# Kernel optimization log

Hardware: AMD Instinct MI355X
Metric: run time of the kernel (lower is better)

## Reference

```python
import jax, jax.numpy as jnp
import numpy as np

N = 8192
E = 262144
C = 256          # in_channels
OUT = 256        # out_channels
H = 4            # num_heads
DH = C // H      # head dim


def setup_inputs() -> dict:
    key = jax.random.key(0)
    ks = jax.random.split(key, 12)
    stdv = 1.0 / np.sqrt(C)
    inp = {
        "x": jax.random.normal(ks[0], (N, C), dtype=jnp.float32),
        "adj": jax.random.randint(ks[1], (2, E), 0, N, dtype=jnp.int64),
        "weight_local": jax.random.uniform(ks[2], (C, C), jnp.float32, -stdv, stdv),
        # nn.MultiheadAttention packed projections
        "in_proj_w": jax.random.normal(ks[3], (3 * C, C), jnp.float32) * stdv,
        "in_proj_b": jnp.zeros((3 * C,), jnp.float32),
        "out_proj_w": jax.random.normal(ks[4], (C, C), jnp.float32) * stdv,
        "out_proj_b": jnp.zeros((C,), jnp.float32),
        "ln_g": jnp.ones((C,), jnp.float32),
        "ln_b": jnp.zeros((C,), jnp.float32),
        "alpha": jnp.zeros((), jnp.float32),
        "fc_w": jax.random.normal(ks[5], (OUT, C), jnp.float32) * stdv,
        "fc_b": jnp.zeros((OUT,), jnp.float32),
    }
    return inp


def _gcn_conv(x, edge_index):
    # out[col] += (1/sqrt(d[col]*d[row])) * x[row], d = in-degree by col
    row, col = edge_index[0], edge_index[1]
    n = x.shape[0]
    d = jax.ops.segment_sum(jnp.ones((edge_index.shape[1],), x.dtype), col, num_segments=n)
    val = jax.lax.rsqrt(d[col] * d[row])
    val = jnp.where(jnp.isfinite(val), val, 0.0)
    msg = x[row] * val[:, None]                      # [E, C] gather + scale
    return jax.ops.segment_sum(msg, col, num_segments=n)  # [N, C] scatter-add


def _mha(x, in_proj_w, in_proj_b, out_proj_w, out_proj_b):
    # single-batch self-attention over all N nodes
    qkv = x @ in_proj_w.T + in_proj_b                # [N, 3C]
    q, k, v = jnp.split(qkv, 3, axis=-1)
    def heads(t):
        return t.reshape(N, H, DH).transpose(1, 0, 2)  # [H, N, DH]
    q, k, v = heads(q), heads(k), heads(v)
    scores = jnp.einsum("hnd,hmd->hnm", q, k) / np.sqrt(DH)  # [H, N, N]
    attn = jax.nn.softmax(scores, axis=-1)
    out = jnp.einsum("hnm,hmd->hnd", attn, v)        # [H, N, DH]
    out = out.transpose(1, 0, 2).reshape(N, C)
    return out @ out_proj_w.T + out_proj_b


def _layernorm(x, g, b, eps=1e-5):
    mu = jnp.mean(x, axis=-1, keepdims=True)
    var = jnp.var(x, axis=-1, keepdims=True)
    return (x - mu) * jax.lax.rsqrt(var + eps) * g + b


def reference(x, adj, weight_local, in_proj_w, in_proj_b, out_proj_w, out_proj_b,
              ln_g, ln_b, alpha, fc_w, fc_b):
    hi = _gcn_conv(x, adj)
    local_embed = hi @ weight_local                   # [N, C]
    attn_out = _mha(x, in_proj_w, in_proj_b, out_proj_w, out_proj_b)
    global_embed = _layernorm(x + attn_out, ln_g, ln_b)
    w = jax.nn.sigmoid(alpha)
    combined = w * local_embed + (1.0 - w) * global_embed
    return combined @ fc_w.T + fc_b                   # [N, OUT]
```

## Files before the change

### kernel.cpp

```cpp
#include <hip/hip_runtime.h>
#include <hip/hip_bf16.h>
#include <math.h>

#define NN   8192
#define EE   262144
#define CC   256
#define HH   4

typedef __bf16 bf16;
typedef __bf16 bf16x8 __attribute__((ext_vector_type(8)));
typedef __bf16 bf16x4 __attribute__((ext_vector_type(4)));
typedef __bf16 bf16x2 __attribute__((ext_vector_type(2)));
typedef float  f32x4  __attribute__((ext_vector_type(4)));

static __device__ __forceinline__ bf16 f2bf(float f) { return (bf16)f; }

static __device__ __forceinline__ unsigned pk2(float a, float b) {
    __hip_bfloat162 h = __float22bfloat162_rn(float2{a, b});
    return *reinterpret_cast<unsigned*>(&h);
}

__global__ void prep_all(const float* __restrict__ x, bf16* __restrict__ xb,
                         const float* __restrict__ ipw, const float* __restrict__ opw,
                         const float* __restrict__ fcw, const float* __restrict__ wloc,
                         bf16* __restrict__ ipwb, bf16* __restrict__ opwb,
                         bf16* __restrict__ fcwb, bf16* __restrict__ wlTb,
                         const int* __restrict__ adj, int* __restrict__ ideg) {
    int b = blockIdx.x, t = threadIdx.x;
    if (b < 2048) {
        for (int i = b * 256 + t; i < NN * CC; i += 2048 * 256) xb[i] = f2bf(x[i]);
    } else if (b < 2816) { int i = (b - 2048) * 256 + t; ipwb[i] = f2bf(ipw[i]); }
    else if (b < 3072)   { int i = (b - 2816) * 256 + t; opwb[i] = f2bf(opw[i]); }
    else if (b < 3328)   { int i = (b - 3072) * 256 + t; fcwb[i] = f2bf(fcw[i]); }
    else if (b < 3584)   { int n = b - 3328;             wlTb[n * 256 + t] = f2bf(wloc[t * 256 + n]); }
    else {
        int e = (b - 3584) * 256 + t;
        if (e < EE) atomicAdd(&ideg[adj[EE + e]], 1);
    }
}

__global__ __launch_bounds__(256) void build_kv(const bf16* __restrict__ qkv,
                                                bf16* __restrict__ Kpk,
                                                bf16* __restrict__ Vpk) {
    __shared__ bf16 tl[64][72];
    const int bx = blockIdx.x;
    const int h  = blockIdx.y;
    const int tid = threadIdx.x;
    #pragma unroll
    for (int i = 0; i < 2; i++) {
        int u = tid + i * 256;
        int key = u >> 3, g = u & 7;
        *reinterpret_cast<bf16x8*>(&tl[key][g * 8]) =
            *reinterpret_cast<const bf16x8*>(qkv + (size_t)(bx * 64 + key) * 768 + 256 + h * 64 + g * 8);
    }
    __syncthreads();
    #pragma unroll
    for (int i = 0; i < 2; i++) {
        int ee = tid + i * 256;
        int l15 = ee & 15, quad = (ee >> 4) & 3, c = (ee >> 6) & 1, ktl = ee >> 7;
        int key_local = (ktl >> 1) * 32 + (l15 >> 2) * 8 + (ktl & 1) * 4 + (l15 & 3);
        bf16x8 v = *reinterpret_cast<const bf16x8*>(&tl[key_local][c * 32 + quad * 8]);
        *reinterpret_cast<bf16x8*>(Kpk + ((size_t)((h * 512 + bx * 4 + ktl) * 2 + c)) * 512
                                       + (quad * 16 + l15) * 8) = v;
    }
    __syncthreads();
    #pragma unroll
    for (int i = 0; i < 2; i++) {
        int u = tid + i * 256;
        int key = u >> 3, g = u & 7;
        *reinterpret_cast<bf16x8*>(&tl[key][g * 8]) =
            *reinterpret_cast<const bf16x8*>(qkv + (size_t)(bx * 64 + key) * 768 + 512 + h * 64 + g * 8);
    }
    __syncthreads();
    #pragma unroll
    for (int i = 0; i < 2; i++) {
        int ee = tid + i * 256;
        int l15 = ee & 15, quad = (ee >> 4) & 3, nt = (ee >> 6) & 3, kcl = ee >> 8;
        bf16x8 v;
        #pragma unroll
        for (int j = 0; j < 8; j++) v[j] = tl[kcl * 32 + quad * 8 + j][nt * 16 + l15];
        *reinterpret_cast<bf16x8*>(Vpk + ((size_t)((h * 256 + bx * 2 + kcl) * 4 + nt)) * 512
                                       + (quad * 16 + l15) * 8) = v;
    }
}

__global__ __launch_bounds__(256) void scan_offsets(const int* __restrict__ ideg,
        int* __restrict__ off, int* __restrict__ cursor, float* __restrict__ rs) {
    __shared__ int ps[256];
    const int tid = threadIdx.x;
    const int base = tid * 32;
    int loc[32];
    int s = 0;
    #pragma unroll
    for (int i = 0; i < 32; i++) { loc[i] = s; s += ideg[base + i]; }
    ps[tid] = s;
    __syncthreads();
    for (int d = 1; d < 256; d <<= 1) {
        int v = (tid >= d) ? ps[tid - d] : 0;
        __syncthreads();
        ps[tid] += v;
        __syncthreads();
    }
    int excl = ps[tid] - s;
    #pragma unroll
    for (int i = 0; i < 32; i++) {
        int o = excl + loc[i];
        off[base + i] = o;
        cursor[base + i] = o;
        int dg = ideg[base + i];
        rs[base + i] = dg > 0 ? rsqrtf((float)dg) : 0.f;
    }
    if (tid == 255) off[8192] = excl + s;
}

__global__ void fill_csr(const int* __restrict__ adj, int* __restrict__ cursor,
                         int* __restrict__ csr) {
    int e = blockIdx.x * 256 + threadIdx.x;
    if (e < EE) {
        int col = adj[EE + e];
        int pos = atomicAdd(&cursor[col], 1);
        csr[pos] = adj[e];
    }
}

__global__ __launch_bounds__(256) void gcn_gather2(const bf16* __restrict__ xb,
        const int* __restrict__ csr, const int* __restrict__ off,
        const float* __restrict__ rs, bf16* __restrict__ hib) {
    const int col = blockIdx.x;
    const int t = threadIdx.x;
    const int half = t >> 7;
    const int j = t & 127;
    const int o = off[col];
    const int cnt = off[col + 1] - o;
    const float rsc = rs[col];
    float a0 = 0.f, a1 = 0.f;
    for (int e = half; e < cnt; e += 2) {
        int r = csr[o + e];
        float v = rsc * rs[r];
        unsigned u = ((const unsigned*)(xb + (size_t)r * CC))[j];
        a0 += __uint_as_float(u << 16) * v;
        a1 += __uint_as_float(u & 0xffff0000u) * v;
    }
    __shared__ float red[512];
    red[half * 256 + 2 * j]     = a0;
    red[half * 256 + 2 * j + 1] = a1;
    __syncthreads();
    if (t < 128) {
        float s0 = red[2 * t]     + red[256 + 2 * t];
        float s1 = red[2 * t + 1] + red[256 + 2 * t + 1];
        bf16x2 pk; pk[0] = f2bf(s0); pk[1] = f2bf(s1);
        ((bf16x2*)(hib + (size_t)col * CC))[t] = pk;
    }
}

__global__ __launch_bounds__(256) void gemm_bt(
        const bf16* __restrict__ A, const bf16* __restrict__ W,
        const float* __restrict__ bias,
        float* __restrict__ outF, bf16* __restrict__ outB,
        int M, int N, int K) {
    const int tid  = threadIdx.x;
    const int wave = tid >> 6;
    const int lane = tid & 63;
    const int quad = lane >> 4;
    const int l15  = lane & 15;
    const int m0 = blockIdx.x * 128;
    const int n0 = blockIdx.y * 64;

    __shared__ bf16 Alds[128][72];
    __shared__ bf16 Wlds[64][72];

    f32x4 acc[2][4];
    #pragma unroll
    for (int mt = 0; mt < 2; mt++)
        #pragma unroll
        for (int nt = 0; nt < 4; nt++)
            acc[mt][nt] = (f32x4){0.f, 0.f, 0.f, 0.f};

    for (int k0 = 0; k0 < K; k0 += 64) {
        #pragma unroll
        for (int i = 0; i < 4; i++) {
            int u = tid + i * 256;
            int r = u >> 3;
            int cp = u & 7;
            *reinterpret_cast<bf16x8*>(&Alds[r][cp * 8]) =
                *reinterpret_cast<const bf16x8*>(A + (size_t)(m0 + r) * K + k0 + cp * 8);
        }
        #pragma unroll
        for (int i = 0; i < 2; i++) {
            int u = tid + i * 256;
            int r = u >> 3;
            int cp = u & 7;
            *reinterpret_cast<bf16x8*>(&Wlds[r][cp * 8]) =
                *reinterpret_cast<const bf16x8*>(W + (size_t)(n0 + r) * K + k0 + cp * 8);
        }
        __syncthreads();
        #pragma unroll
        for (int c = 0; c < 2; c++) {
            bf16x8 af[2], wf[4];
            #pragma unroll
            for (int mt = 0; mt < 2; mt++)
                af[mt] = *reinterpret_cast<const bf16x8*>(&Alds[wave * 32 + mt * 16 + l15][c * 32 + quad * 8]);
            #pragma unroll
            for (int nt = 0; nt < 4; nt++)
                wf[nt] = *reinterpret_cast<const bf16x8*>(&Wlds[nt * 16 + l15][c * 32 + quad * 8]);
            #pragma unroll
            for (int mt = 0; mt < 2; mt++)
                #pragma unroll
                for (int nt = 0; nt < 4; nt++)
                    acc[mt][nt] = __builtin_amdgcn_mfma_f32_16x16x32_bf16(af[mt], wf[nt], acc[mt][nt], 0, 0, 0);
        }
        __syncthreads();
    }
    #pragma unroll
    for (int mt = 0; mt < 2; mt++)
        #pragma unroll
        for (int nt = 0; nt < 4; nt++)
            #pragma unroll
            for (int r = 0; r < 4; r++) {
                int m = m0 + wave * 32 + mt * 16 + quad * 4 + r;
                int n = n0 + nt * 16 + l15;
                float v = acc[mt][nt][r];
                if (bias) v += bias[n];
                if (outF) outF[(size_t)m * N + n] = v;
                else      outB[(size_t)m * N + n] = f2bf(v);
            }
}

__global__ __launch_bounds__(256, 3) void flash_attn7(const bf16* __restrict__ qkv,
                                                      const bf16* __restrict__ Kpk,
                                                      const bf16* __restrict__ Vpk,
                                                      bf16* __restrict__ Opart,
                                                      float* __restrict__ lpart) {
    const int tid  = threadIdx.x;
    const int w    = tid >> 6;
    const int lane = tid & 63;
    const int quad = lane >> 4;
    const int l15  = lane & 15;
    const int bx = blockIdx.x;
    const int h    = bx & 3;
    const int qb   = (bx >> 2) & 127;
    const int half = bx >> 9;
    const int qbase = qb * 64;

    __shared__ bf16 Osh[4][64][68];
    __shared__ float lsh[4][64];

    const float qs = 0.180336880f;
    bf16x8 qf[4][2];
    #pragma unroll
    for (int qt = 0; qt < 4; qt++)
        #pragma unroll
        for (int c = 0; c < 2; c++) {
            bf16x8 raw = *reinterpret_cast<const bf16x8*>(
                qkv + (size_t)(qbase + qt * 16 + l15) * 768 + h * 64 + c * 32 + quad * 8);
            #pragma unroll
            for (int j = 0; j < 8; j++) qf[qt][c][j] = f2bf((float)raw[j] * qs);
        }

    const bf16* Kb = Kpk + (size_t)h * 524288 + lane * 8;
    const bf16* Vb = Vpk + (size_t)h * 524288 + lane * 8;
    const int cbase = half * 128 + w;

    f32x4 oacc[4][4];
    #pragma unroll
    for (int qt = 0; qt < 4; qt++)
        #pragma unroll
        for (int nt = 0; nt < 4; nt++) oacc[qt][nt] = (f32x4){0.f, 0.f, 0.f, 0.f};
    f32x4 lacc[4];
    #pragma unroll
    for (int qt = 0; qt < 4; qt++) lacc[qt] = (f32x4){0.f, 0.f, 0.f, 0.f};
    bf16x8 onesf;
    #pragma unroll
    for (int j = 0; j < 8; j++) onesf[j] = f2bf(1.0f);
    const f32x4 z4 = (f32x4){0.f, 0.f, 0.f, 0.f};

    for (int i = 0; i < 32; i++) {
        const int kc = cbase + i * 4;
        bf16x8 kf[2][2], vf[4];
        #pragma unroll
        for (int s = 0; s < 2; s++)
            #pragma unroll
            for (int c = 0; c < 2; c++)
                kf[s][c] = *reinterpret_cast<const bf16x8*>(Kb + kc * 2048 + s * 1024 + c * 512);
        #pragma unroll
        for (int nt = 0; nt < 4; nt++)
            vf[nt] = *reinterpret_cast<const bf16x8*>(Vb + kc * 2048 + nt * 512);

        f32x4 sacc[2][4];
        #pragma unroll
        for (int s = 0; s < 2; s++)
            #pragma unroll
            for (int qt = 0; qt < 4; qt++) {
                sacc[s][qt] = __builtin_amdgcn_mfma_f32_16x16x32_bf16(kf[s][0], qf[qt][0], z4, 0, 0, 0);
                sacc[s][qt] = __builtin_amdgcn_mfma_f32_16x16x32_bf16(kf[s][1], qf[qt][1], sacc[s][qt], 0, 0, 0);
            }
        #pragma unroll
        for (int qt = 0; qt < 4; qt++) {
            float e0 = __builtin_amdgcn_exp2f(sacc[0][qt][0]);
            float e1 = __builtin_amdgcn_exp2f(sacc[0][qt][1]);
            float e2 = __builtin_amdgcn_exp2f(sacc[0][qt][2]);
            float e3 = __builtin_amdgcn_exp2f(sacc[0][qt][3]);
            float e4 = __builtin_amdgcn_exp2f(sacc[1][qt][0]);
            float e5 = __builtin_amdgcn_exp2f(sacc[1][qt][1]);
            float e6 = __builtin_amdgcn_exp2f(sacc[1][qt][2]);
            float e7 = __builtin_amdgcn_exp2f(sacc[1][qt][3]);
            union { bf16x8 v; unsigned u[4]; } pu;
            pu.u[0] = pk2(e0, e1);
            pu.u[1] = pk2(e2, e3);
            pu.u[2] = pk2(e4, e5);
            pu.u[3] = pk2(e6, e7);
            #pragma unroll
            for (int nt = 0; nt < 4; nt++)
                oacc[qt][nt] = __builtin_amdgcn_mfma_f32_16x16x32_bf16(pu.v, vf[nt], oacc[qt][nt], 0, 0, 0);
            lacc[qt] = __builtin_amdgcn_mfma_f32_16x16x32_bf16(pu.v, onesf, lacc[qt], 0, 0, 0);
        }
    }

    #pragma unroll
    for (int qt = 0; qt < 4; qt++)
        #pragma unroll
        for (int nt = 0; nt < 4; nt++)
            #pragma unroll
            for (int r = 0; r < 4; r++)
                Osh[w][qt * 16 + quad * 4 + r][nt * 16 + l15] = f2bf(oacc[qt][nt][r]);
    if (l15 == 0) {
        #pragma unroll
        for (int qt = 0; qt < 4; qt++)
            #pragma unroll
            for (int r = 0; r < 4; r++)
                lsh[w][qt * 16 + quad * 4 + r] = lacc[qt][r];
    }
    __syncthreads();

    const int q = w * 16 + l15;
    const size_t ob = (size_t)half * 2097152 + ((size_t)(h * 128 + qb) * 64 + q) * 64;
    if (quad == 0)
        lpart[half * 32768 + (h * 128 + qb) * 64 + q] =
            lsh[0][q] + lsh[1][q] + lsh[2][q] + lsh[3][q];
    #pragma unroll
    for (int gg = 0; gg < 4; gg++) {
        int d0 = gg * 16 + quad * 4;
        f32x4 acc = (f32x4){0.f, 0.f, 0.f, 0.f};
        #pragma unroll
        for (int v = 0; v < 4; v++) {
            bf16x4 ov = *reinterpret_cast<const bf16x4*>(&Osh[v][q][d0]);
            #pragma unroll
            for (int i = 0; i < 4; i++) acc[i] += (float)ov[i];
        }
        bf16x4 obv;
        #pragma unroll
        for (int i = 0; i < 4; i++) obv[i] = f2bf(acc[i]);
        *reinterpret_cast<bf16x4*>(Opart + ob + d0) = obv;
    }
}

__global__ __launch_bounds__(256) void attn_merge(const bf16* __restrict__ Opart,
                                                  const float* __restrict__ lpart,
                                                  bf16* __restrict__ attnO) {
    const int b = blockIdx.x;
    const int h = b >> 7;
    const int qb = b & 127;
    const int t = threadIdx.x;
    const int q = t >> 2;
    const int dg = t & 3;
    const float linv = 1.f / (lpart[b * 64 + q] + lpart[32768 + b * 64 + q]);
    const bf16* p0 = Opart + ((size_t)b * 64 + q) * 64 + dg * 16;
    const bf16* p1 = p0 + 2097152;
    bf16x8 a0 = *reinterpret_cast<const bf16x8*>(p0);
    bf16x8 a1 = *reinterpret_cast<const bf16x8*>(p0 + 8);
    bf16x8 b0 = *reinterpret_cast<const bf16x8*>(p1);
    bf16x8 b1 = *reinterpret_cast<const bf16x8*>(p1 + 8);
    bf16x8 o0, o1;
    #pragma unroll
    for (int i = 0; i < 8; i++) {
        o0[i] = f2bf(((float)a0[i] + (float)b0[i]) * linv);
        o1[i] = f2bf(((float)a1[i] + (float)b1[i]) * linv);
    }
    bf16* dst = attnO + (size_t)(qb * 64 + q) * CC + h * 64 + dg * 16;
    *reinterpret_cast<bf16x8*>(dst) = o0;
    *reinterpret_cast<bf16x8*>(dst + 8) = o1;
}

__global__ __launch_bounds__(256) void ln_combine2(
        const float* __restrict__ x, const float* __restrict__ aproj,
        const float* __restrict__ local, const float* __restrict__ g,
        const float* __restrict__ b, const float* __restrict__ alpha_p,
        bf16* __restrict__ comb) {
    const int row = blockIdx.x * 4 + (threadIdx.x >> 6);
    const int lane = threadIdx.x & 63;
    const f32x4 xv = ((const f32x4*)(x + (size_t)row * CC))[lane];
    const f32x4 av = ((const f32x4*)(aproj + (size_t)row * CC))[lane];
    f32x4 v = xv + av;
    float s = v[0] + v[1] + v[2] + v[3];
    #pragma unroll
    for (int off = 1; off < 64; off <<= 1) s += __shfl_xor(s, off);
    float mu = s * (1.f / CC);
    f32x4 d = v - mu;
    float ss = d[0] * d[0] + d[1] * d[1] + d[2] * d[2] + d[3] * d[3];
    #pragma unroll
    for (int off = 1; off < 64; off <<= 1) ss += __shfl_xor(ss, off);
    float rstd = rsqrtf(ss * (1.f / CC) + 1e-5f);
    const f32x4 gv = ((const f32x4*)g)[lane];
    const f32x4 bv = ((const f32x4*)b)[lane];
    const f32x4 lv = ((const f32x4*)(local + (size_t)row * CC))[lane];
    float wgt = 1.f / (1.f + __expf(-alpha_p[0]));
    bf16x4 o;
    #pragma unroll
    for (int i = 0; i < 4; i++)
        o[i] = f2bf(wgt * lv[i] + (1.f - wgt) * (d[i] * rstd * gv[i] + bv[i]));
    ((bf16x4*)(comb + (size_t)row * CC))[lane] = o;
}

extern "C" void kernel_launch(void* const* d_in, const int* in_sizes, int n_in,
                              void* d_out, int out_size, void* d_ws, size_t ws_size,
                              hipStream_t stream) {
    (void)in_sizes; (void)n_in; (void)out_size; (void)ws_size;
    const float* x    = (const float*)d_in[0];
    const int*   adj  = (const int*)d_in[1];
    const float* wloc = (const float*)d_in[2];
    const float* ipw  = (const float*)d_in[3];
    const float* ipb  = (const float*)d_in[4];
    const float* opw  = (const float*)d_in[5];
    const float* opb  = (const float*)d_in[6];
    const float* lng  = (const float*)d_in[7];
    const float* lnb  = (const float*)d_in[8];
    const float* alp  = (const float*)d_in[9];
    const float* fcw  = (const float*)d_in[10];
    const float* fcb  = (const float*)d_in[11];
    float* out = (float*)d_out;

    char* p = (char*)d_ws;
    int*   ideg   = (int*)p;    p += (size_t)NN * 4;
    int*   off    = (int*)p;    p += (size_t)(NN + 1) * 4;
    int*   cursor = (int*)p;    p += (size_t)NN * 4;
    float* rs     = (float*)p;  p += (size_t)NN * 4;
    int*   csr    = (int*)p;    p += (size_t)EE * 4;
    bf16* xb    = (bf16*)p;   p += (size_t)NN * CC * 2;
    bf16* hib   = (bf16*)p;   p += (size_t)NN * CC * 2;
    bf16* ipwb  = (bf16*)p;   p += (size_t)768 * 256 * 2;
    bf16* wlTb  = (bf16*)p;   p += (size_t)256 * 256 * 2;
    bf16* opwb  = (bf16*)p;   p += (size_t)256 * 256 * 2;
    bf16* fcwb  = (bf16*)p;   p += (size_t)256 * 256 * 2;
    bf16* qkvb  = (bf16*)p;   p += (size_t)NN * 768 * 2;
    bf16* Kpk   = (bf16*)p;   p += (size_t)HH * 512 * 2 * 512 * 2;
    bf16* Vpk   = (bf16*)p;   p += (size_t)HH * 256 * 4 * 512 * 2;
    bf16* aOb   = (bf16*)p;   p += (size_t)NN * CC * 2;
    float* aprj = (float*)p;  p += (size_t)NN * CC * 4;
    float* locl = (float*)p;  p += (size_t)NN * CC * 4;
    bf16* comb  = (bf16*)p;   p += (size_t)NN * CC * 2;
    bf16*  Opart = (bf16*)aprj;
    float* lpart = (float*)locl;

    hipMemsetAsync(ideg, 0, (size_t)NN * 4, stream);

    prep_all<<<4608, 256, 0, stream>>>(x, xb, ipw, opw, fcw, wloc, ipwb, opwb, fcwb, wlTb, adj, ideg);
    scan_offsets<<<1, 256, 0, stream>>>(ideg, off, cursor, rs);
    fill_csr<<<EE / 256, 256, 0, stream>>>(adj, cursor, csr);
    gcn_gather2<<<NN, 256, 0, stream>>>(xb, csr, off, rs, hib);

    gemm_bt<<<dim3(NN / 128, 768 / 64), 256, 0, stream>>>(xb, ipwb, ipb, nullptr, qkvb, NN, 768, 256);
    build_kv<<<dim3(NN / 64, HH), 256, 0, stream>>>(qkvb, Kpk, Vpk);
    flash_attn7<<<1024, 256, 0, stream>>>(qkvb, Kpk, Vpk, Opart, lpart);
    attn_merge<<<512, 256, 0, stream>>>(Opart, lpart, aOb);
    gemm_bt<<<dim3(NN / 128, 256 / 64), 256, 0, stream>>>(aOb, opwb, opb, aprj, nullptr, NN, 256, 256);
    gemm_bt<<<dim3(NN / 128, 256 / 64), 256, 0, stream>>>(hib, wlTb, nullptr, locl, nullptr, NN, 256, 256);
    ln_combine2<<<NN / 4, 256, 0, stream>>>(x, aprj, locl, lng, lnb, alp, comb);
    gemm_bt<<<dim3(NN / 128, 256 / 64), 256, 0, stream>>>(comb, fcwb, fcb, out, nullptr, NN, 256, 256);
}
```

Measured before the change: 310.0 us.

## Halve attention query tile, write head-interleaved partials, merge two GEMMs into one launch

New measurement: 305.0 us. Within noise of the previous version (-1.6%).

```diff
diff --git a/kernel.cpp b/kernel.cpp
--- a/kernel.cpp
+++ b/kernel.cpp
@@ -153,11 +153,11 @@
     }
 }
 
-__global__ __launch_bounds__(256) void gemm_bt(
+static __device__ __forceinline__ void gemm_core(
         const bf16* __restrict__ A, const bf16* __restrict__ W,
         const float* __restrict__ bias,
         float* __restrict__ outF, bf16* __restrict__ outB,
-        int M, int N, int K) {
+        int M, int N, int K, bf16 (*Alds)[72], bf16 (*Wlds)[72]) {
     const int tid  = threadIdx.x;
     const int wave = tid >> 6;
     const int lane = tid & 63;
@@ -165,9 +165,6 @@
     const int l15  = lane & 15;
     const int m0 = blockIdx.x * 128;
     const int n0 = blockIdx.y * 64;
-
-    __shared__ bf16 Alds[128][72];
-    __shared__ bf16 Wlds[64][72];
 
     f32x4 acc[2][4];
     #pragma unroll
@@ -226,7 +223,28 @@
             }
 }
 
-__global__ __launch_bounds__(256, 3) void flash_attn7(const bf16* __restrict__ qkv,
+__global__ __launch_bounds__(256) void gemm_bt(
+        const bf16* __restrict__ A, const bf16* __restrict__ W,
+        const float* __restrict__ bias,
+        float* __restrict__ outF, bf16* __restrict__ outB,
+        int M, int N, int K) {
+    __shared__ bf16 Alds[128][72];
+    __shared__ bf16 Wlds[64][72];
+    gemm_core(A, W, bias, outF, outB, M, N, K, Alds, Wlds);
+}
+
+__global__ __launch_bounds__(256) void gemm_dual(
+        const bf16* __restrict__ A0, const bf16* __restrict__ W0,
+        const float* __restrict__ b0, float* __restrict__ o0,
+        const bf16* __restrict__ A1, const bf16* __restrict__ W1,
+        float* __restrict__ o1) {
+    __shared__ bf16 Alds[128][72];
+    __shared__ bf16 Wlds[64][72];
+    if (blockIdx.z == 0) gemm_core(A0, W0, b0, o0, nullptr, NN, 256, 256, Alds, Wlds);
+    else                 gemm_core(A1, W1, nullptr, o1, nullptr, NN, 256, 256, Alds, Wlds);
+}
+
+__global__ __launch_bounds__(256, 4) void flash_attn9(const bf16* __restrict__ qkv,
                                                       const bf16* __restrict__ Kpk,
                                                       const bf16* __restrict__ Vpk,
                                                       bf16* __restrict__ Opart,
@@ -238,17 +256,17 @@
     const int l15  = lane & 15;
     const int bx = blockIdx.x;
     const int h    = bx & 3;
-    const int qb   = (bx >> 2) & 127;
-    const int half = bx >> 9;
-    const int qbase = qb * 64;
-
-    __shared__ bf16 Osh[4][64][68];
-    __shared__ float lsh[4][64];
+    const int qb   = (bx >> 2) & 255;
+    const int half = bx >> 10;
+    const int qbase = qb * 32;
+
+    __shared__ bf16 Osh[4][32][68];
+    __shared__ float lsh[4][32];
 
     const float qs = 0.180336880f;
-    bf16x8 qf[4][2];
-    #pragma unroll
-    for (int qt = 0; qt < 4; qt++)
+    bf16x8 qf[2][2];
+    #pragma unroll
+    for (int qt = 0; qt < 2; qt++)
         #pragma unroll
         for (int c = 0; c < 2; c++) {
             bf16x8 raw = *reinterpret_cast<const bf16x8*>(
@@ -261,14 +279,14 @@
     const bf16* Vb = Vpk + (size_t)h * 524288 + lane * 8;
     const int cbase = half * 128 + w;
 
-    f32x4 oacc[4][4];
-    #pragma unroll
-    for (int qt = 0; qt < 4; qt++)
+    f32x4 oacc[2][4];
+    #pragma unroll
+    for (int qt = 0; qt < 2; qt++)
         #pragma unroll
         for (int nt = 0; nt < 4; nt++) oacc[qt][nt] = (f32x4){0.f, 0.f, 0.f, 0.f};
-    f32x4 lacc[4];
-    #pragma unroll
-    for (int qt = 0; qt < 4; qt++) lacc[qt] = (f32x4){0.f, 0.f, 0.f, 0.f};
+    f32x4 lacc[2];
+    #pragma unroll
+    for (int qt = 0; qt < 2; qt++) lacc[qt] = (f32x4){0.f, 0.f, 0.f, 0.f};
     bf16x8 onesf;
     #pragma unroll
     for (int j = 0; j < 8; j++) onesf[j] = f2bf(1.0f);
@@ -286,16 +304,16 @@
         for (int nt = 0; nt < 4; nt++)
             vf[nt] = *reinterpret_cast<const bf16x8*>(Vb + kc * 2048 + nt * 512);
 
-        f32x4 sacc[2][4];
+        f32x4 sacc[2][2];
         #pragma unroll
         for (int s = 0; s < 2; s++)
             #pragma unroll
-            for (int qt = 0; qt < 4; qt++) {
+            for (int qt = 0; qt < 2; qt++) {
                 sacc[s][qt] = __builtin_amdgcn_mfma_f32_16x16x32_bf16(kf[s][0], qf[qt][0], z4, 0, 0, 0);
                 sacc[s][qt] = __builtin_amdgcn_mfma_f32_16x16x32_bf16(kf[s][1], qf[qt][1], sacc[s][qt], 0, 0, 0);
             }
         #pragma unroll
-        for (int qt = 0; qt < 4; qt++) {
+        for (int qt = 0; qt < 2; qt++) {
             float e0 = __builtin_amdgcn_exp2f(sacc[0][qt][0]);
             float e1 = __builtin_amdgcn_exp2f(sacc[0][qt][1]);
             float e2 = __builtin_amdgcn_exp2f(sacc[0][qt][2]);
@@ -317,7 +335,7 @@
     }
 
     #pragma unroll
-    for (int qt = 0; qt < 4; qt++)
+    for (int qt = 0; qt < 2; qt++)
         #pragma unroll
         for (int nt = 0; nt < 4; nt++)
             #pragma unroll
@@ -325,46 +343,44 @@
                 Osh[w][qt * 16 + quad * 4 + r][nt * 16 + l15] = f2bf(oacc[qt][nt][r]);
     if (l15 == 0) {
         #pragma unroll
-        for (int qt = 0; qt < 4; qt++)
+        for (int qt = 0; qt < 2; qt++)
             #pragma unroll
             for (int r = 0; r < 4; r++)
                 lsh[w][qt * 16 + quad * 4 + r] = lacc[qt][r];
     }
     __syncthreads();
 
-    const int q = w * 16 + l15;
-    const size_t ob = (size_t)half * 2097152 + ((size_t)(h * 128 + qb) * 64 + q) * 64;
-    if (quad == 0)
-        lpart[half * 32768 + (h * 128 + qb) * 64 + q] =
-            lsh[0][q] + lsh[1][q] + lsh[2][q] + lsh[3][q];
-    #pragma unroll
-    for (int gg = 0; gg < 4; gg++) {
-        int d0 = gg * 16 + quad * 4;
-        f32x4 acc = (f32x4){0.f, 0.f, 0.f, 0.f};
-        #pragma unroll
-        for (int v = 0; v < 4; v++) {
-            bf16x4 ov = *reinterpret_cast<const bf16x4*>(&Osh[v][q][d0]);
-            #pragma unroll
-            for (int i = 0; i < 4; i++) acc[i] += (float)ov[i];
-        }
-        bf16x4 obv;
-        #pragma unroll
-        for (int i = 0; i < 4; i++) obv[i] = f2bf(acc[i]);
-        *reinterpret_cast<bf16x4*>(Opart + ob + d0) = obv;
-    }
+    const int q32 = tid >> 3;
+    const int dg = tid & 7;
+    const int d0 = dg * 8;
+    float acc[8];
+    #pragma unroll
+    for (int i = 0; i < 8; i++) acc[i] = 0.f;
+    #pragma unroll
+    for (int v = 0; v < 4; v++) {
+        bf16x8 ov = *reinterpret_cast<const bf16x8*>(&Osh[v][q32][d0]);
+        #pragma unroll
+        for (int i = 0; i < 8; i++) acc[i] += (float)ov[i];
+    }
+    bf16x8 ob;
+    #pragma unroll
+    for (int i = 0; i < 8; i++) ob[i] = f2bf(acc[i]);
+    *reinterpret_cast<bf16x8*>(Opart + (size_t)half * 2097152
+                               + (size_t)(qbase + q32) * 256 + h * 64 + d0) = ob;
+    if (dg == 0)
+        lpart[((half << 2) + h) * 8192 + qbase + q32] =
+            lsh[0][q32] + lsh[1][q32] + lsh[2][q32] + lsh[3][q32];
 }
 
 __global__ __launch_bounds__(256) void attn_merge(const bf16* __restrict__ Opart,
                                                   const float* __restrict__ lpart,
                                                   bf16* __restrict__ attnO) {
-    const int b = blockIdx.x;
-    const int h = b >> 7;
-    const int qb = b & 127;
     const int t = threadIdx.x;
-    const int q = t >> 2;
-    const int dg = t & 3;
-    const float linv = 1.f / (lpart[b * 64 + q] + lpart[32768 + b * 64 + q]);
-    const bf16* p0 = Opart + ((size_t)b * 64 + q) * 64 + dg * 16;
+    const int q = blockIdx.x * 16 + (t >> 4);
+    const int c0 = (t & 15) * 16;
+    const int h = c0 >> 6;
+    const float linv = 1.f / (lpart[h * 8192 + q] + lpart[(4 + h) * 8192 + q]);
+    const bf16* p0 = Opart + (size_t)q * 256 + c0;
     const bf16* p1 = p0 + 2097152;
     bf16x8 a0 = *reinterpret_cast<const bf16x8*>(p0);
     bf16x8 a1 = *reinterpret_cast<const bf16x8*>(p0 + 8);
@@ -376,7 +392,7 @@
         o0[i] = f2bf(((float)a0[i] + (float)b0[i]) * linv);
         o1[i] = f2bf(((float)a1[i] + (float)b1[i]) * linv);
     }
-    bf16* dst = attnO + (size_t)(qb * 64 + q) * CC + h * 64 + dg * 16;
+    bf16* dst = attnO + (size_t)q * CC + c0;
     *reinterpret_cast<bf16x8*>(dst) = o0;
     *reinterpret_cast<bf16x8*>(dst + 8) = o1;
 }
@@ -460,10 +476,9 @@
 
     gemm_bt<<<dim3(NN / 128, 768 / 64), 256, 0, stream>>>(xb, ipwb, ipb, nullptr, qkvb, NN, 768, 256);
     build_kv<<<dim3(NN / 64, HH), 256, 0, stream>>>(qkvb, Kpk, Vpk);
-    flash_attn7<<<1024, 256, 0, stream>>>(qkvb, Kpk, Vpk, Opart, lpart);
+    flash_attn9<<<2048, 256, 0, stream>>>(qkvb, Kpk, Vpk, Opart, lpart);
     attn_merge<<<512, 256, 0, stream>>>(Opart, lpart, aOb);
-    gemm_bt<<<dim3(NN / 128, 256 / 64), 256, 0, stream>>>(aOb, opwb, opb, aprj, nullptr, NN, 256, 256);
-    gemm_bt<<<dim3(NN / 128, 256 / 64), 256, 0, stream>>>(hib, wlTb, nullptr, locl, nullptr, NN, 256, 256);
+    gemm_dual<<<dim3(NN / 128, 4, 2), 256, 0, stream>>>(aOb, opwb, opb, aprj, hib, wlTb, locl);
     ln_combine2<<<NN / 4, 256, 0, stream>>>(x, aprj, locl, lng, lnb, alp, comb);
     gemm_bt<<<dim3(NN / 128, 256 / 64), 256, 0, stream>>>(comb, fcwb, fcb, out, nullptr, NN, 256, 256);
 }
```
